# Performance work log

Measured on AMD Instinct MI355X. Metric: run time of the kernel, lower is better.

Reference implementation:

```python
import jax, jax.numpy as jnp
import numpy as np

TAU = 1.0  # temperaturesa
GRID = 5   # torch.chunk(..., 5) along H and W


def _cam(X, gamma, tau):
    # Channel attention: energy = Xf Xf^T over spatial dim, with max-subtraction/negation trick.
    B, C, H, W = X.shape
    Xf = X.reshape(B, C, H * W)
    energy = jnp.einsum('bcn,bdn->bcd', Xf, Xf)                      # [B,C,C]
    energy_new = jnp.max(energy, axis=-1, keepdims=True) - energy
    attn = jax.nn.softmax(energy_new / tau, axis=-1)
    out = jnp.einsum('bcd,bdn->bcn', attn, Xf).reshape(B, C, H, W)
    return gamma * out + X


def _pam(X, Wq, bq, Wk, bk, Wv, bv, gamma, tau):
    # Position attention with 1x1-conv q/k/v (1x1 conv == channel matmul).
    B, C, H, W = X.shape
    N = H * W
    Xf = X.reshape(B, C, N)
    q = jnp.einsum('kc,bcn->bnk', Wq, Xf) + bq                        # [B,N,C//8]
    k = jnp.einsum('kc,bcn->bkn', Wk, Xf) + bk[None, :, None]         # [B,C//8,N]
    v = jnp.einsum('dc,bcn->bdn', Wv, Xf) + bv[None, :, None]         # [B,C,N]
    energy = jnp.einsum('bnk,bkm->bnm', q, k)                         # [B,N,N]
    attn = jax.nn.softmax(energy / tau, axis=-1)
    # torch: bmm(value, attention.permute(0,2,1)) -> out[b,d,m] = sum_n v[b,d,n]*attn[b,m,n]
    out = jnp.einsum('bdn,bmn->bdm', v, attn).reshape(B, C, H, W)
    return gamma * out + X


def _cka_loss(X, Y):
    # linear_CKA_loss: HKH centering done as K - rowmean - colmean + totalmean.
    def cgram(Z):
        K = Z @ Z.T                                                   # [B,B]
        rm = jnp.mean(K, axis=1, keepdims=True)
        cm = jnp.mean(K, axis=0, keepdims=True)
        return K - rm - cm + jnp.mean(K)
    cX, cY = cgram(X), cgram(Y)
    hsic = jnp.sum(cX * cY)
    v1 = jnp.sqrt(jnp.sum(cX * cX))
    v2 = jnp.sqrt(jnp.sum(cY * cY))
    return -jnp.log(jnp.abs(hsic / (v1 * v2)) + 1e-8)


def _grid_chunks(X, g=GRID):
    # 5x5 spatial tiling -> [g*g, B, C, H/g, W/g]
    B, C, H, W = X.shape
    h, w = H // g, W // g
    return X.reshape(B, C, g, h, g, w).transpose(2, 4, 0, 1, 3, 5).reshape(g * g, B, C, h, w)


def setup_inputs() -> dict:
    key = jax.random.key(0)
    ks = jax.random.split(key, 10)
    B, C, H, W = 16, 256, 80, 80
    Ck = C // 8
    return {
        'feat_S': jax.random.normal(ks[0], (B, C, H, W), jnp.float32),
        'feat_T': jax.random.normal(ks[1], (B, C, H, W), jnp.float32),
        'Wq': jax.random.normal(ks[2], (Ck, C), jnp.float32),
        'bq': jax.random.normal(ks[3], (Ck,), jnp.float32),
        'Wk': jax.random.normal(ks[4], (Ck, C), jnp.float32),
        'bk': jax.random.normal(ks[5], (Ck,), jnp.float32),
        'Wv': jax.random.normal(ks[6], (C, C), jnp.float32),
        'bv': jax.random.normal(ks[7], (C,), jnp.float32),
        'gammacam': jax.random.normal(ks[8], (1,), jnp.float32),
        'gammapam': jax.random.normal(ks[9], (1,), jnp.float32),
    }


def reference(feat_S, feat_T, Wq, bq, Wk, bk, Wv, bv, gammacam, gammapam):
    # feature_transform == 'separately_CAMgridPAM_CKA'
    tau = TAU
    pam = lambda X: _pam(X, Wq, bq, Wk, bk, Wv, bv, gammapam, tau)
    chunks_S = _grid_chunks(feat_S)                                   # [25,B,C,16,16]
    chunks_T = _grid_chunks(feat_T)
    pam_S = jax.vmap(pam)(chunks_S)
    pam_T = jax.vmap(pam)(chunks_T)
    nchunk, B = pam_S.shape[0], pam_S.shape[1]
    flat_S = pam_S.reshape(nchunk, B, -1)
    flat_T = pam_T.reshape(nchunk, B, -1)
    loss_PAM = jnp.mean(jax.vmap(_cka_loss)(flat_S, flat_T))          # sum/n == mean
    CAM_S = _cam(feat_S, gammacam, tau)
    CAM_T = _cam(feat_T, gammacam, tau)
    loss_CAM = _cka_loss(CAM_S.reshape(B, -1), CAM_T.reshape(B, -1))
    return (loss_CAM, loss_PAM)
```

## Files before the change

### kernel.cpp

```cpp
#include <hip/hip_runtime.h>


typedef short bf16x8 __attribute__((ext_vector_type(8)));
typedef float f32x4 __attribute__((ext_vector_type(4)));

constexpr int BB = 16;
constexpr int CH = 256;
constexpr int HW = 6400;
constexpr int IMW = 80;

__device__ __forceinline__ int lds_off(int row, int half, int k2) {
  return row * 128 + ((((half << 6)) | k2) ^ ((row & 7) << 4));
}

__device__ __forceinline__ bf16x8 frag_ld(const char* base, int row, int half, int lane) {
  int off = row * 128 + ((((half << 6)) | ((lane >> 4) << 4)) ^ ((lane & 7) << 4));
  return *(const bf16x8*)(base + off);
}

__device__ __forceinline__ void cvt2(float x, unsigned short& h, unsigned short& l) {
  unsigned u = __float_as_uint(x);
  h = (unsigned short)(u >> 16);
  float r = x - __uint_as_float(u & 0xffff0000u);
  l = (unsigned short)(__float_as_uint(r) >> 16);
}

__device__ __forceinline__ void cvt4(float4 v, ushort4& h, ushort4& l) {
  cvt2(v.x, h.x, l.x); cvt2(v.y, h.y, l.y);
  cvt2(v.z, h.z, l.z); cvt2(v.w, h.w, l.w);
}

__device__ __forceinline__ void cvt8(float4 v0, float4 v1, bf16x8& hi, bf16x8& lo) {
  unsigned short h, l;
  cvt2(v0.x, h, l); hi[0] = (short)h; lo[0] = (short)l;
  cvt2(v0.y, h, l); hi[1] = (short)h; lo[1] = (short)l;
  cvt2(v0.z, h, l); hi[2] = (short)h; lo[2] = (short)l;
  cvt2(v0.w, h, l); hi[3] = (short)h; lo[3] = (short)l;
  cvt2(v1.x, h, l); hi[4] = (short)h; lo[4] = (short)l;
  cvt2(v1.y, h, l); hi[5] = (short)h; lo[5] = (short)l;
  cvt2(v1.z, h, l); hi[6] = (short)h; lo[6] = (short)l;
  cvt2(v1.w, h, l); hi[7] = (short)h; lo[7] = (short)l;
}

__device__ __forceinline__ unsigned short bf_rnd(float x) {
  unsigned u = __float_as_uint(x);
  return (unsigned short)((u + 0x8000u) >> 16);
}

__global__ __launch_bounds__(1024) void cam_energy_k(const float* __restrict__ fS,
                                                     const float* __restrict__ fT,
                                                     float* __restrict__ part) {
  const int kc = blockIdx.x, b = blockIdx.y, t = blockIdx.z;
  const float* X = (t ? fT : fS) + (size_t)b * CH * HW;
  __shared__ unsigned short lds[2 * 256 * 64];
  const int tid = threadIdx.x, lane = tid & 63, w = tid >> 6;
  const int wr = w >> 2, wc = w & 3;
  const int r0 = tid >> 2, kq = tid & 3;
  const int half = kq >> 1, k2b = (kq & 1) * 32;
  const float* Xr = X + (size_t)r0 * HW + kc * 800 + kq * 16;
  f32x4 acc[4][4] = {};
  float4 v[4];
#pragma unroll
  for (int q = 0; q < 4; ++q) v[q] = *(const float4*)(Xr + q * 4);
  for (int it = 0; it < 13; ++it) {
    char* pb = (char*)lds + (it & 1) * 32768;
#pragma unroll
    for (int q = 0; q < 4; ++q) {
      ushort4 u;
      u.x = bf_rnd(v[q].x); u.y = bf_rnd(v[q].y);
      u.z = bf_rnd(v[q].z); u.w = bf_rnd(v[q].w);
      *(ushort4*)(pb + lds_off(r0, half, k2b + q * 8)) = u;
    }
    __syncthreads();
    float4 nv[4];
    if (it < 12) {
      const int nk = (it + 1) * 64;
      if (nk + kq * 16 < 800) {
        const float* Xn = Xr + nk;
#pragma unroll
        for (int q = 0; q < 4; ++q) nv[q] = *(const float4*)(Xn + q * 4);
      } else {
#pragma unroll
        for (int q = 0; q < 4; ++q) nv[q] = make_float4(0.f, 0.f, 0.f, 0.f);
      }
    }
#pragma unroll
    for (int h = 0; h < 2; ++h) {
      bf16x8 bh[4];
#pragma unroll
      for (int n = 0; n < 4; ++n)
        bh[n] = frag_ld(pb, wc * 64 + n * 16 + (lane & 15), h, lane);
#pragma unroll
      for (int m = 0; m < 4; ++m) {
        bf16x8 a = frag_ld(pb, wr * 64 + m * 16 + (lane & 15), h, lane);
#pragma unroll
        for (int n = 0; n < 4; ++n)
          acc[m][n] = __builtin_amdgcn_mfma_f32_16x16x32_bf16(a, bh[n], acc[m][n], 0, 0, 0);
      }
    }
#pragma unroll
    for (int q = 0; q < 4; ++q) v[q] = nv[q];
  }
  float* Eb = part + (((size_t)kc * 2 + t) * BB + b) * 65536;
#pragma unroll
  for (int m = 0; m < 4; ++m)
#pragma unroll
    for (int n = 0; n < 4; ++n) {
      int row = wr * 64 + m * 16 + ((lane >> 4) << 2);
      int col = wc * 64 + n * 16 + (lane & 15);
#pragma unroll
      for (int r2 = 0; r2 < 4; ++r2)
        Eb[(size_t)(row + r2) * 256 + col] = acc[m][n][r2];
    }
}

__global__ __launch_bounds__(64) void cam_softmax_k(float* __restrict__ part) {
  const int c = blockIdx.x, b = blockIdx.y, t = blockIdx.z;
  const size_t base = (((size_t)t * BB + b) * CH + c) * CH;
  const int lane = threadIdx.x;
  float4 x = make_float4(0.f, 0.f, 0.f, 0.f);
#pragma unroll
  for (int p = 0; p < 8; ++p) {
    float4 y = ((const float4*)(part + (size_t)p * 2097152 + base))[lane];
    x.x += y.x; x.y += y.y; x.z += y.z; x.w += y.w;
  }
  float mn = fminf(fminf(x.x, x.y), fminf(x.z, x.w));
  for (int o = 32; o; o >>= 1) mn = fminf(mn, __shfl_xor(mn, o));
  float4 p4;
  p4.x = __expf(mn - x.x); p4.y = __expf(mn - x.y);
  p4.z = __expf(mn - x.z); p4.w = __expf(mn - x.w);
  float s = (p4.x + p4.y) + (p4.z + p4.w);
  for (int o = 32; o; o >>= 1) s += __shfl_xor(s, o);
  const float inv = 1.0f / s;
  p4.x *= inv; p4.y *= inv; p4.z *= inv; p4.w *= inv;
  ((float4*)(part + base))[lane] = p4;
}

template <int MODE>
__global__ __launch_bounds__(1024) void ax_k(const float* __restrict__ Abase, int Astride,
                                             const float* __restrict__ X,
                                             float* __restrict__ OUT,
                                             const float* __restrict__ bvec,
                                             const float* __restrict__ gsc) {
  const int nt = blockIdx.x;
  const int b = blockIdx.y;
  const float* A = Abase + (size_t)b * Astride;
  const float* Xb = X + (size_t)b * CH * HW;
  float* OUTb = OUT + (size_t)b * CH * HW;
  const int nbase = nt * 128;
  __shared__ unsigned short lds[2 * (256 + 128) * 64];
  const int tid = threadIdx.x, lane = tid & 63, w = tid >> 6;
  const int wr = w >> 2, wc = w & 3;
  const int r0 = tid >> 2, kq = tid & 3;
  const int n_r = tid & 127, kg = tid >> 7;
  const float* Xcol = Xb + nbase + n_r;
  f32x4 acc[4][2] = {};
  float4 ra[2];
  float vb4[4];
#pragma unroll
  for (int q = 0; q < 2; ++q)
    ra[q] = *(const float4*)(A + (size_t)r0 * 256 + kq * 8 + q * 4);
#pragma unroll
  for (int e = 0; e < 4; ++e)
    vb4[e] = Xcol[(size_t)(kg * 4 + e) * HW];
  for (int s = 0; s < 8; ++s) {
    char* Ab = (char*)lds + (s & 1) * 49152;
    char* Bb = Ab + 32768;
#pragma unroll
    for (int q = 0; q < 2; ++q) {
      ushort4 h4, l4;
      cvt4(ra[q], h4, l4);
      *(ushort4*)(Ab + lds_off(r0, 0, kq * 16 + q * 8)) = h4;
      *(ushort4*)(Ab + lds_off(r0, 1, kq * 16 + q * 8)) = l4;
    }
    {
      unsigned short bh[4], bl[4];
#pragma unroll
      for (int e = 0; e < 4; ++e) cvt2(vb4[e], bh[e], bl[e]);
      *(ushort4*)(Bb + lds_off(n_r, 0, kg * 8)) = make_ushort4(bh[0], bh[1], bh[2], bh[3]);
      *(ushort4*)(Bb + lds_off(n_r, 1, kg * 8)) = make_ushort4(bl[0], bl[1], bl[2], bl[3]);
    }
    __syncthreads();
    if (s < 7) {
      int k0 = (s + 1) * 32;
#pragma unroll
      for (int q = 0; q < 2; ++q)
        ra[q] = *(const float4*)(A + (size_t)r0 * 256 + k0 + kq * 8 + q * 4);
#pragma unroll
      for (int e = 0; e < 4; ++e)
        vb4[e] = Xcol[(size_t)(k0 + kg * 4 + e) * HW];
    }
    bf16x8 bfr[2][2];
#pragma unroll
    for (int h = 0; h < 2; ++h)
#pragma unroll
      for (int n = 0; n < 2; ++n)
        bfr[h][n] = frag_ld(Bb, wc * 32 + n * 16 + (lane & 15), h, lane);
#pragma unroll
    for (int m = 0; m < 4; ++m) {
      int arow = wr * 64 + m * 16 + (lane & 15);
      bf16x8 a0 = frag_ld(Ab, arow, 0, lane);
      bf16x8 a1 = frag_ld(Ab, arow, 1, lane);
#pragma unroll
      for (int n = 0; n < 2; ++n)
        acc[m][n] = __builtin_amdgcn_mfma_f32_16x16x32_bf16(a0, bfr[0][n], acc[m][n], 0, 0, 0);
#pragma unroll
      for (int n = 0; n < 2; ++n)
        acc[m][n] = __builtin_amdgcn_mfma_f32_16x16x32_bf16(a0, bfr[1][n], acc[m][n], 0, 0, 0);
#pragma unroll
      for (int n = 0; n < 2; ++n)
        acc[m][n] = __builtin_amdgcn_mfma_f32_16x16x32_bf16(a1, bfr[0][n], acc[m][n], 0, 0, 0);
    }
  }
  float g = 0.f;
  if (MODE == 0) g = gsc[0];
#pragma unroll
  for (int m = 0; m < 4; ++m)
#pragma unroll
    for (int n = 0; n < 2; ++n) {
      int row = wr * 64 + m * 16 + ((lane >> 4) << 2);
      int col = nbase + wc * 32 + n * 16 + (lane & 15);
#pragma unroll
      for (int r2 = 0; r2 < 4; ++r2) {
        size_t o = (size_t)(row + r2) * HW + col;
        float v = acc[m][n][r2];
        if (MODE == 0) OUTb[o] = g * v + Xb[o];
        else           OUTb[o] = v + bvec[row + r2];
      }
    }
}

__global__ __launch_bounds__(256) void qk_k(const float* __restrict__ X,
                                            const float* __restrict__ Wq,
                                            const float* __restrict__ bq,
                                            const float* __restrict__ Wk,
                                            const float* __restrict__ bk,
                                            float* __restrict__ qt,
                                            float* __restrict__ kf) {
  const int nbase = blockIdx.x * 256;
  const int b = blockIdx.y;
  const float* Xb = X + (size_t)b * CH * HW;
  __shared__ unsigned short lds[(64 + 256) * 64];
  char* Ab = (char*)lds;
  char* Bb = (char*)lds + 8192;
  const int tid = threadIdx.x, lane = tid & 63, w = tid >> 6;
  const int ar = tid >> 2, akq = tid & 3;
  const int n4 = (tid & 63) * 4, c0l = tid >> 6;
  const float* Arow = (ar < 32) ? (Wq + (size_t)ar * CH) : (Wk + (size_t)(ar - 32) * CH);
  f32x4 acc[4][4] = {};
  float4 va[2], vb[8];
#pragma unroll
  for (int q = 0; q < 2; ++q)
    va[q] = *(const float4*)(Arow + akq * 8 + q * 4);
#pragma unroll
  for (int q = 0; q < 8; ++q)
    vb[q] = *(const float4*)(Xb + (size_t)(c0l + 4 * q) * HW + nbase + n4);
  for (int s = 0; s < 8; ++s) {
    __syncthreads();
#pragma unroll
    for (int q = 0; q < 2; ++q) {
      ushort4 h4, l4;
      cvt4(va[q], h4, l4);
      *(ushort4*)(Ab + lds_off(ar, 0, akq * 16 + q * 8)) = h4;
      *(ushort4*)(Ab + lds_off(ar, 1, akq * 16 + q * 8)) = l4;
    }
#pragma unroll
    for (int q = 0; q < 8; ++q) {
      int cc = c0l + 4 * q;
      float4 v = vb[q];
#pragma unroll
      for (int jj = 0; jj < 4; ++jj) {
        int j = (jj + tid) & 3;
        float e = (j == 0) ? v.x : (j == 1) ? v.y : (j == 2) ? v.z : v.w;
        unsigned short h, l;
        cvt2(e, h, l);
        int row = n4 + j;
        *(unsigned short*)(Bb + lds_off(row, 0, cc * 2)) = h;
        *(unsigned short*)(Bb + lds_off(row, 1, cc * 2)) = l;
      }
    }
    __syncthreads();
    float4 na[2], nb[8];
    if (s < 7) {
      const int k0 = (s + 1) * 32;
#pragma unroll
      for (int q = 0; q < 2; ++q)
        na[q] = *(const float4*)(Arow + k0 + akq * 8 + q * 4);
#pragma unroll
      for (int q = 0; q < 8; ++q)
        nb[q] = *(const float4*)(Xb + (size_t)(k0 + c0l + 4 * q) * HW + nbase + n4);
    }
    bf16x8 bfr[2][4];
#pragma unroll
    for (int h = 0; h < 2; ++h)
#pragma unroll
      for (int n = 0; n < 4; ++n)
        bfr[h][n] = frag_ld(Bb, w * 64 + n * 16 + (lane & 15), h, lane);
#pragma unroll
    for (int m = 0; m < 4; ++m) {
      int arow2 = m * 16 + (lane & 15);
      bf16x8 a0 = frag_ld(Ab, arow2, 0, lane);
      bf16x8 a1 = frag_ld(Ab, arow2, 1, lane);
#pragma unroll
      for (int n = 0; n < 4; ++n)
        acc[m][n] = __builtin_amdgcn_mfma_f32_16x16x32_bf16(a0, bfr[0][n], acc[m][n], 0, 0, 0);
#pragma unroll
      for (int n = 0; n < 4; ++n)
        acc[m][n] = __builtin_amdgcn_mfma_f32_16x16x32_bf16(a0, bfr[1][n], acc[m][n], 0, 0, 0);
#pragma unroll
      for (int n = 0; n < 4; ++n)
        acc[m][n] = __builtin_amdgcn_mfma_f32_16x16x32_bf16(a1, bfr[0][n], acc[m][n], 0, 0, 0);
    }
#pragma unroll
    for (int q = 0; q < 2; ++q) va[q] = na[q];
#pragma unroll
    for (int q = 0; q < 8; ++q) vb[q] = nb[q];
  }
#pragma unroll
  for (int m = 0; m < 4; ++m)
#pragma unroll
    for (int n = 0; n < 4; ++n) {
      int row = m * 16 + ((lane >> 4) << 2);
      int col = nbase + w * 64 + n * 16 + (lane & 15);
#pragma unroll
      for (int r2 = 0; r2 < 4; ++r2) {
        int rr = row + r2;
        float v = acc[m][n][r2];
        if (rr < 32) qt[((size_t)b * HW + col) * 32 + rr] = v + bq[rr];
        else         kf[((size_t)b * 32 + (rr - 32)) * HW + col] = v + bk[rr - 32];
      }
    }
}

__global__ __launch_bounds__(256) void pam_es_k(const float* __restrict__ qt,
                                                const float* __restrict__ kf,
                                                float* __restrict__ Pbuf) {
  const int ccb = blockIdx.x;
  const int ck = ccb >> 4, b = ccb & 15;
  const int gi = ck / 5, gj = ck % 5;
  const int pbase = gi * 16 * IMW + gj * 16;
  float* Pc = Pbuf + (size_t)ccb * 65536;
  __shared__ float qs[256][32];
  __shared__ float S[32][256];
  const int tid = threadIdx.x;
  const float* qb = qt + (size_t)b * HW * 32;
#pragma unroll
  for (int qq = 0; qq < 8; ++qq) {
    int j = (tid >> 3) + 32 * qq;
    int nj = pbase + (j >> 4) * IMW + (j & 15);
    float4 v = *(const float4*)(qb + (size_t)nj * 32 + (tid & 7) * 4);
    *(float4*)&qs[j][(tid & 7) * 4] = v;
  }
  const int nt = pbase + (tid >> 4) * IMW + (tid & 15);
  const float* kb = kf + (size_t)b * 32 * HW;
  float kc[32];
#pragma unroll
  for (int kk = 0; kk < 32; ++kk) kc[kk] = kb[(size_t)kk * HW + nt];
  __syncthreads();
  const int w = tid >> 6, lane = tid & 63;
  for (int p = 0; p < 8; ++p) {
#pragma unroll 4
    for (int j2 = 0; j2 < 32; ++j2) {
      int row = p * 32 + j2;
      float s = 0.f;
#pragma unroll
      for (int k8 = 0; k8 < 8; ++k8) {
        float4 qv = *(const float4*)&qs[row][k8 * 4];
        s = fmaf(qv.x, kc[k8 * 4 + 0], s);
        s = fmaf(qv.y, kc[k8 * 4 + 1], s);
        s = fmaf(qv.z, kc[k8 * 4 + 2], s);
        s = fmaf(qv.w, kc[k8 * 4 + 3], s);
      }
      S[j2][tid] = s;
    }
    __syncthreads();
#pragma unroll
    for (int rr = 0; rr < 8; ++rr) {
      int jj = w * 8 + rr;
      float4 v = *(const float4*)&S[jj][lane << 2];
      float m = fmaxf(fmaxf(v.x, v.y), fmaxf(v.z, v.w));
      for (int o = 32; o; o >>= 1) m = fmaxf(m, __shfl_xor(m, o));
      float4 pv;
      pv.x = __expf(v.x - m); pv.y = __expf(v.y - m);
      pv.z = __expf(v.z - m); pv.w = __expf(v.w - m);
      float s = (pv.x + pv.y) + (pv.z + pv.w);
      for (int o = 32; o; o >>= 1) s += __shfl_xor(s, o);
      const float inv = 1.f / s;
      pv.x *= inv; pv.y *= inv; pv.z *= inv; pv.w *= inv;
      *(float4*)&Pc[(size_t)(p * 32 + jj) * 256 + (lane << 2)] = pv;
    }
    __syncthreads();
  }
}

__global__ __launch_bounds__(1024) void pam_pv_k(float* __restrict__ P,
                                                 const float* __restrict__ V,
                                                 const float* __restrict__ fS,
                                                 const float* __restrict__ fT,
                                                 const float* __restrict__ gsc, int t) {
  const int ccb = blockIdx.x;
  const int ck = ccb >> 4, b = ccb & 15;
  const int gi = ck / 5, gj = ck % 5;
  const float* Xb = (t ? fT : fS) + (size_t)b * CH * HW;
  const float* Vb = V + (size_t)b * CH * HW;
  float* Pc = P + (size_t)ccb * 65536;
  __shared__ unsigned short lds[2 * 2 * 256 * 64];
  const int tid = threadIdx.x, lane = tid & 63, w = tid >> 6;
  const int wr = w >> 2, wc = w & 3;
  const int r0 = tid >> 2, kq = tid & 3;
  const int pbase = gi * 16 * IMW + gj * 16;
  f32x4 acc[4][4] = {};
  float4 va[2], vb[2];
  {
    int jj = kq * 8;
    int ngl = pbase + (jj >> 4) * IMW + (jj & 15);
    va[0] = *(const float4*)(Vb + (size_t)r0 * HW + ngl);
    va[1] = *(const float4*)(Vb + (size_t)r0 * HW + ngl + 4);
    vb[0] = *(const float4*)(Pc + (size_t)r0 * 256 + jj);
    vb[1] = *(const float4*)(Pc + (size_t)r0 * 256 + jj + 4);
  }
  for (int s = 0; s < 8; ++s) {
    char* Ab = (char*)lds + (s & 1) * 65536;
    char* Bb = Ab + 32768;
    {
      ushort4 h4, l4;
      cvt4(va[0], h4, l4);
      *(ushort4*)(Ab + lds_off(r0, 0, kq * 16)) = h4;
      *(ushort4*)(Ab + lds_off(r0, 1, kq * 16)) = l4;
      cvt4(va[1], h4, l4);
      *(ushort4*)(Ab + lds_off(r0, 0, kq * 16 + 8)) = h4;
      *(ushort4*)(Ab + lds_off(r0, 1, kq * 16 + 8)) = l4;
      cvt4(vb[0], h4, l4);
      *(ushort4*)(Bb + lds_off(r0, 0, kq * 16)) = h4;
      *(ushort4*)(Bb + lds_off(r0, 1, kq * 16)) = l4;
      cvt4(vb[1], h4, l4);
      *(ushort4*)(Bb + lds_off(r0, 0, kq * 16 + 8)) = h4;
      *(ushort4*)(Bb + lds_off(r0, 1, kq * 16 + 8)) = l4;
    }
    __syncthreads();
    if (s < 7) {
      int k0 = (s + 1) * 32;
      int jj = k0 + kq * 8;
      int ngl = pbase + (jj >> 4) * IMW + (jj & 15);
      va[0] = *(const float4*)(Vb + (size_t)r0 * HW + ngl);
      va[1] = *(const float4*)(Vb + (size_t)r0 * HW + ngl + 4);
      vb[0] = *(const float4*)(Pc + (size_t)r0 * 256 + k0 + kq * 8);
      vb[1] = *(const float4*)(Pc + (size_t)r0 * 256 + k0 + kq * 8 + 4);
    }
#pragma unroll
    for (int hb = 0; hb < 2; ++hb) {
      bf16x8 bh[4];
#pragma unroll
      for (int n = 0; n < 4; ++n)
        bh[n] = frag_ld(Bb, wc * 64 + n * 16 + (lane & 15), hb, lane);
#pragma unroll
      for (int m = 0; m < 4; ++m) {
        int arow = wr * 64 + m * 16 + (lane & 15);
        bf16x8 a0 = frag_ld(Ab, arow, 0, lane);
#pragma unroll
        for (int n = 0; n < 4; ++n)
          acc[m][n] = __builtin_amdgcn_mfma_f32_16x16x32_bf16(a0, bh[n], acc[m][n], 0, 0, 0);
        if (hb == 0) {
          bf16x8 a1 = frag_ld(Ab, arow, 1, lane);
#pragma unroll
          for (int n = 0; n < 4; ++n)
            acc[m][n] = __builtin_amdgcn_mfma_f32_16x16x32_bf16(a1, bh[n], acc[m][n], 0, 0, 0);
        }
      }
    }
  }
  const float g = gsc[0];
#pragma unroll
  for (int m = 0; m < 4; ++m)
#pragma unroll
    for (int n = 0; n < 4; ++n) {
      int row = wr * 64 + m * 16 + ((lane >> 4) << 2);
      int col = wc * 64 + n * 16 + (lane & 15);
      int ngl = pbase + (col >> 4) * IMW + (col & 15);
#pragma unroll
      for (int r2 = 0; r2 < 4; ++r2) {
        float v = g * acc[m][n][r2] + Xb[(size_t)(row + r2) * HW + ngl];
        Pc[(size_t)(row + r2) * 256 + col] = v;
      }
    }
}

__global__ __launch_bounds__(256) void gram_mfma_k(const float* __restrict__ Z,
                                                   size_t gStride, size_t bStride,
                                                   double* __restrict__ G) {
  const int tid = threadIdx.x, lane = tid & 63, w = tid >> 6;
  const float* Zg = Z + (size_t)blockIdx.y * gStride;
  const float* p = Zg + (size_t)(lane & 15) * bStride +
                   (size_t)blockIdx.x * 4096 + w * 1024 + ((lane >> 4) << 3);
  f32x4 acc = {};
#pragma unroll 4
  for (int s = 0; s < 32; ++s) {
    float4 v0 = *(const float4*)(p + s * 32);
    float4 v1 = *(const float4*)(p + s * 32 + 4);
    bf16x8 hi, lo;
    cvt8(v0, v1, hi, lo);
    acc = __builtin_amdgcn_mfma_f32_16x16x32_bf16(hi, hi, acc, 0, 0, 0);
    acc = __builtin_amdgcn_mfma_f32_16x16x32_bf16(hi, lo, acc, 0, 0, 0);
    acc = __builtin_amdgcn_mfma_f32_16x16x32_bf16(lo, hi, acc, 0, 0, 0);
  }
  double* Gt = G + (size_t)blockIdx.y * 256;
  const int col = lane & 15, row0 = (lane >> 4) << 2;
#pragma unroll
  for (int i = 0; i < 4; ++i)
    atomicAdd(&Gt[(size_t)(row0 + i) * 16 + col], (double)acc[i]);
}

__global__ __launch_bounds__(256) void cka_pair_k(const double* __restrict__ G,
                                                  double* __restrict__ losses) {
  const int q = blockIdx.x;
  const double* KX = (q == 0) ? G : G + 512 + (size_t)(q - 1) * 256;
  const double* KY = (q == 0) ? G + 256 : G + 512 + 6400 + (size_t)(q - 1) * 256;
  __shared__ double red[256];
  __shared__ double srm[16], scm[16];
  __shared__ double stm;
  const int tid = threadIdx.x;
  const int r = tid >> 4, c = tid & 15;

  auto center = [&](double k) -> double {
    red[tid] = k;
    __syncthreads();
    for (int off = 8; off; off >>= 1) {
      if (c < off) red[tid] += red[tid + off];
      __syncthreads();
    }
    if (c == 0) srm[r] = red[tid] * (1.0 / 16.0);
    __syncthreads();
    red[c * 16 + r] = k;
    __syncthreads();
    for (int off = 8; off; off >>= 1) {
      if (r < off) red[c * 16 + r] += red[c * 16 + r + off];
      __syncthreads();
    }
    if (r == 0) scm[c] = red[c * 16] * (1.0 / 16.0);
    __syncthreads();
    if (tid == 0) {
      double s = 0.0;
      for (int i = 0; i < 16; ++i) s += srm[i];
      stm = s * (1.0 / 16.0);
    }
    __syncthreads();
    double v = k - srm[r] - scm[c] + stm;
    __syncthreads();
    return v;
  };
  auto reduce_sum = [&](double v) -> double {
    red[tid] = v;
    __syncthreads();
    for (int off = 128; off; off >>= 1) {
      if (tid < off) red[tid] += red[tid + off];
      __syncthreads();
    }
    double s = red[0];
    __syncthreads();
    return s;
  };
  double cx = center(KX[tid]);
  double cy = center(KY[tid]);
  double h = reduce_sum(cx * cy);
  double v1 = reduce_sum(cx * cx);
  double v2 = reduce_sum(cy * cy);
  if (tid == 0) losses[q] = -log(fabs(h / (sqrt(v1) * sqrt(v2))) + 1e-8);
}

__global__ void cka_combine_k(const double* __restrict__ losses,
                              float* __restrict__ out) {
  if (threadIdx.x == 0) {
    out[0] = (float)losses[0];
    double s = 0.0;
    for (int q = 1; q <= 25; ++q) s += losses[q];
    out[1] = (float)(s * (1.0 / 25.0));
  }
}

extern "C" void kernel_launch(void* const* d_in, const int* in_sizes, int n_in,
                              void* d_out, int out_size, void* d_ws, size_t ws_size,
                              hipStream_t stream) {
  (void)in_sizes; (void)n_in; (void)out_size; (void)ws_size;
  const float* fS = (const float*)d_in[0];
  const float* fT = (const float*)d_in[1];
  const float* Wq = (const float*)d_in[2];
  const float* bq = (const float*)d_in[3];
  const float* Wk = (const float*)d_in[4];
  const float* bk = (const float*)d_in[5];
  const float* Wv = (const float*)d_in[6];
  const float* bv = (const float*)d_in[7];
  const float* gcam = (const float*)d_in[8];
  const float* gpam = (const float*)d_in[9];
  float* out = (float*)d_out;

  float* buf0 = (float*)d_ws;
  float* buf1 = buf0 + 26214400;
  double* G = (double*)(buf1 + 26214400);
  float* Pbuf = buf1;
  float* qt = buf0;
  float* kf = buf0 + 3276800;
  double* losses = (double*)buf0;

  hipMemsetAsync(G, 0, 13312 * sizeof(double), stream);

  cam_energy_k<<<dim3(8, 16, 2), 1024, 0, stream>>>(fS, fT, buf1);
  cam_softmax_k<<<dim3(256, 16, 2), 64, 0, stream>>>(buf1);
  for (int t = 0; t < 2; ++t) {
    ax_k<0><<<dim3(50, 16), 1024, 0, stream>>>(buf1 + (size_t)t * BB * 65536, 65536,
                                               t ? fT : fS, buf0, nullptr, gcam);
    gram_mfma_k<<<dim3(400, 1), 256, 0, stream>>>(buf0, (size_t)0, (size_t)1638400,
                                                  G + t * 256);
  }
  for (int t = 0; t < 2; ++t) {
    const float* X = t ? fT : fS;
    qk_k<<<dim3(25, 16), 256, 0, stream>>>(X, Wq, bq, Wk, bk, qt, kf);
    pam_es_k<<<dim3(400), 256, 0, stream>>>(qt, kf, Pbuf);
    ax_k<1><<<dim3(50, 16), 1024, 0, stream>>>(Wv, 0, X, buf0, bv, nullptr);
    pam_pv_k<<<dim3(400), 1024, 0, stream>>>(Pbuf, buf0, fS, fT, gpam, t);
    gram_mfma_k<<<dim3(16, 25), 256, 0, stream>>>(Pbuf, (size_t)1048576, (size_t)65536,
                                                  G + 512 + t * 6400);
  }
  cka_pair_k<<<dim3(26), 256, 0, stream>>>(G, losses);
  cka_combine_k<<<dim3(1), 64, 0, stream>>>(losses, out);
}
```

Before: 993.5 us.

## Shrink GEMM blocks to 512 threads, single LDS buffer, split PV output columns

ax_k and pam_pv_k now run 512-thread blocks (launch bounds 512,4), with each wave computing a 64x64 tile. The LDS double buffer is replaced by a single buffer guarded by two barriers per k-step, so less shared memory is used per block and more blocks can reside on a CU. pam_pv_k is split into two blocks per chunk, one per half of the output positions, and writes its result in a per-half layout. That layout is a consistent permutation across S and T, so the later Gram computation is unaffected. The intent is to raise occupancy and parallelism, at the cost of losing the overlap between LDS writes and MFMA work and adding an extra barrier per step.

```diff
diff --git a/kernel.cpp b/kernel.cpp
--- a/kernel.cpp
+++ b/kernel.cpp
@@ -137,79 +137,82 @@
 }
 
 template <int MODE>
-__global__ __launch_bounds__(1024) void ax_k(const float* __restrict__ Abase, int Astride,
-                                             const float* __restrict__ X,
-                                             float* __restrict__ OUT,
-                                             const float* __restrict__ bvec,
-                                             const float* __restrict__ gsc) {
+__global__ __launch_bounds__(512, 4) void ax_k(const float* __restrict__ Abase, int Astride,
+                                               const float* __restrict__ X,
+                                               float* __restrict__ OUT,
+                                               const float* __restrict__ bvec,
+                                               const float* __restrict__ gsc) {
   const int nt = blockIdx.x;
   const int b = blockIdx.y;
   const float* A = Abase + (size_t)b * Astride;
   const float* Xb = X + (size_t)b * CH * HW;
   float* OUTb = OUT + (size_t)b * CH * HW;
   const int nbase = nt * 128;
-  __shared__ unsigned short lds[2 * (256 + 128) * 64];
+  __shared__ unsigned short lds[(256 + 128) * 64];
+  char* Ab = (char*)lds;
+  char* Bb = (char*)lds + 32768;
   const int tid = threadIdx.x, lane = tid & 63, w = tid >> 6;
-  const int wr = w >> 2, wc = w & 3;
-  const int r0 = tid >> 2, kq = tid & 3;
+  const int wr = w >> 1, wc = w & 1;
+  const int r0a = tid >> 1, kqa = tid & 1;
   const int n_r = tid & 127, kg = tid >> 7;
   const float* Xcol = Xb + nbase + n_r;
-  f32x4 acc[4][2] = {};
-  float4 ra[2];
-  float vb4[4];
-#pragma unroll
-  for (int q = 0; q < 2; ++q)
-    ra[q] = *(const float4*)(A + (size_t)r0 * 256 + kq * 8 + q * 4);
-#pragma unroll
-  for (int e = 0; e < 4; ++e)
-    vb4[e] = Xcol[(size_t)(kg * 4 + e) * HW];
+  f32x4 acc[4][4] = {};
+  float4 ra[4];
+  float vb8[8];
+#pragma unroll
+  for (int q = 0; q < 4; ++q)
+    ra[q] = *(const float4*)(A + (size_t)r0a * 256 + kqa * 16 + q * 4);
+#pragma unroll
+  for (int e = 0; e < 8; ++e)
+    vb8[e] = Xcol[(size_t)(kg * 8 + e) * HW];
   for (int s = 0; s < 8; ++s) {
-    char* Ab = (char*)lds + (s & 1) * 49152;
-    char* Bb = Ab + 32768;
-#pragma unroll
-    for (int q = 0; q < 2; ++q) {
+    __syncthreads();
+#pragma unroll
+    for (int q = 0; q < 4; ++q) {
       ushort4 h4, l4;
       cvt4(ra[q], h4, l4);
-      *(ushort4*)(Ab + lds_off(r0, 0, kq * 16 + q * 8)) = h4;
-      *(ushort4*)(Ab + lds_off(r0, 1, kq * 16 + q * 8)) = l4;
+      *(ushort4*)(Ab + lds_off(r0a, 0, kqa * 32 + q * 8)) = h4;
+      *(ushort4*)(Ab + lds_off(r0a, 1, kqa * 32 + q * 8)) = l4;
     }
     {
-      unsigned short bh[4], bl[4];
-#pragma unroll
-      for (int e = 0; e < 4; ++e) cvt2(vb4[e], bh[e], bl[e]);
-      *(ushort4*)(Bb + lds_off(n_r, 0, kg * 8)) = make_ushort4(bh[0], bh[1], bh[2], bh[3]);
-      *(ushort4*)(Bb + lds_off(n_r, 1, kg * 8)) = make_ushort4(bl[0], bl[1], bl[2], bl[3]);
+      unsigned short bh[8], bl[8];
+#pragma unroll
+      for (int e = 0; e < 8; ++e) cvt2(vb8[e], bh[e], bl[e]);
+      *(ushort4*)(Bb + lds_off(n_r, 0, kg * 16)) = make_ushort4(bh[0], bh[1], bh[2], bh[3]);
+      *(ushort4*)(Bb + lds_off(n_r, 0, kg * 16 + 8)) = make_ushort4(bh[4], bh[5], bh[6], bh[7]);
+      *(ushort4*)(Bb + lds_off(n_r, 1, kg * 16)) = make_ushort4(bl[0], bl[1], bl[2], bl[3]);
+      *(ushort4*)(Bb + lds_off(n_r, 1, kg * 16 + 8)) = make_ushort4(bl[4], bl[5], bl[6], bl[7]);
     }
     __syncthreads();
     if (s < 7) {
       int k0 = (s + 1) * 32;
 #pragma unroll
-      for (int q = 0; q < 2; ++q)
-        ra[q] = *(const float4*)(A + (size_t)r0 * 256 + k0 + kq * 8 + q * 4);
-#pragma unroll
-      for (int e = 0; e < 4; ++e)
-        vb4[e] = Xcol[(size_t)(k0 + kg * 4 + e) * HW];
-    }
-    bf16x8 bfr[2][2];
-#pragma unroll
-    for (int h = 0; h < 2; ++h)
-#pragma unroll
-      for (int n = 0; n < 2; ++n)
-        bfr[h][n] = frag_ld(Bb, wc * 32 + n * 16 + (lane & 15), h, lane);
-#pragma unroll
-    for (int m = 0; m < 4; ++m) {
-      int arow = wr * 64 + m * 16 + (lane & 15);
-      bf16x8 a0 = frag_ld(Ab, arow, 0, lane);
-      bf16x8 a1 = frag_ld(Ab, arow, 1, lane);
-#pragma unroll
-      for (int n = 0; n < 2; ++n)
-        acc[m][n] = __builtin_amdgcn_mfma_f32_16x16x32_bf16(a0, bfr[0][n], acc[m][n], 0, 0, 0);
-#pragma unroll
-      for (int n = 0; n < 2; ++n)
-        acc[m][n] = __builtin_amdgcn_mfma_f32_16x16x32_bf16(a0, bfr[1][n], acc[m][n], 0, 0, 0);
-#pragma unroll
-      for (int n = 0; n < 2; ++n)
-        acc[m][n] = __builtin_amdgcn_mfma_f32_16x16x32_bf16(a1, bfr[0][n], acc[m][n], 0, 0, 0);
+      for (int q = 0; q < 4; ++q)
+        ra[q] = *(const float4*)(A + (size_t)r0a * 256 + k0 + kqa * 16 + q * 4);
+#pragma unroll
+      for (int e = 0; e < 8; ++e)
+        vb8[e] = Xcol[(size_t)(k0 + kg * 8 + e) * HW];
+    }
+#pragma unroll
+    for (int hb = 0; hb < 2; ++hb) {
+      bf16x8 bh[4];
+#pragma unroll
+      for (int n = 0; n < 4; ++n)
+        bh[n] = frag_ld(Bb, wc * 64 + n * 16 + (lane & 15), hb, lane);
+#pragma unroll
+      for (int m = 0; m < 4; ++m) {
+        int arow = wr * 64 + m * 16 + (lane & 15);
+        bf16x8 a0 = frag_ld(Ab, arow, 0, lane);
+#pragma unroll
+        for (int n = 0; n < 4; ++n)
+          acc[m][n] = __builtin_amdgcn_mfma_f32_16x16x32_bf16(a0, bh[n], acc[m][n], 0, 0, 0);
+        if (hb == 0) {
+          bf16x8 a1 = frag_ld(Ab, arow, 1, lane);
+#pragma unroll
+          for (int n = 0; n < 4; ++n)
+            acc[m][n] = __builtin_amdgcn_mfma_f32_16x16x32_bf16(a1, bh[n], acc[m][n], 0, 0, 0);
+        }
+      }
     }
   }
   float g = 0.f;
@@ -217,9 +220,9 @@
 #pragma unroll
   for (int m = 0; m < 4; ++m)
 #pragma unroll
-    for (int n = 0; n < 2; ++n) {
+    for (int n = 0; n < 4; ++n) {
       int row = wr * 64 + m * 16 + ((lane >> 4) << 2);
-      int col = nbase + wc * 32 + n * 16 + (lane & 15);
+      int col = nbase + wc * 64 + n * 16 + (lane & 15);
 #pragma unroll
       for (int r2 = 0; r2 < 4; ++r2) {
         size_t o = (size_t)(row + r2) * HW + col;
@@ -393,59 +396,67 @@
   }
 }
 
-__global__ __launch_bounds__(1024) void pam_pv_k(float* __restrict__ P,
-                                                 const float* __restrict__ V,
-                                                 const float* __restrict__ fS,
-                                                 const float* __restrict__ fT,
-                                                 const float* __restrict__ gsc, int t) {
-  const int ccb = blockIdx.x;
+__global__ __launch_bounds__(512, 4) void pam_pv_k(float* __restrict__ P,
+                                                   const float* __restrict__ V,
+                                                   const float* __restrict__ fS,
+                                                   const float* __restrict__ fT,
+                                                   const float* __restrict__ gsc, int t) {
+  const int jh = blockIdx.x;
+  const int ccb = blockIdx.y;
   const int ck = ccb >> 4, b = ccb & 15;
   const int gi = ck / 5, gj = ck % 5;
   const float* Xb = (t ? fT : fS) + (size_t)b * CH * HW;
   const float* Vb = V + (size_t)b * CH * HW;
   float* Pc = P + (size_t)ccb * 65536;
-  __shared__ unsigned short lds[2 * 2 * 256 * 64];
+  const float* Pr = Pc + (size_t)jh * 32768;
+  float* Oc = Pc + (size_t)jh * 32768;
+  __shared__ unsigned short lds[(256 + 128) * 64];
+  char* Ab = (char*)lds;
+  char* Bb = (char*)lds + 32768;
   const int tid = threadIdx.x, lane = tid & 63, w = tid >> 6;
-  const int wr = w >> 2, wc = w & 3;
-  const int r0 = tid >> 2, kq = tid & 3;
+  const int wr = w >> 1, wc = w & 1;
+  const int r0a = tid >> 1, kqa = tid & 1;
+  const int r0b = tid >> 2, kqb = tid & 3;
   const int pbase = gi * 16 * IMW + gj * 16;
   f32x4 acc[4][4] = {};
-  float4 va[2], vb[2];
+  float4 va[4], vp[2];
   {
-    int jj = kq * 8;
-    int ngl = pbase + (jj >> 4) * IMW + (jj & 15);
-    va[0] = *(const float4*)(Vb + (size_t)r0 * HW + ngl);
-    va[1] = *(const float4*)(Vb + (size_t)r0 * HW + ngl + 4);
-    vb[0] = *(const float4*)(Pc + (size_t)r0 * 256 + jj);
-    vb[1] = *(const float4*)(Pc + (size_t)r0 * 256 + jj + 4);
+    int jj = kqa * 16;
+    int ngl = pbase + (jj >> 4) * IMW;
+#pragma unroll
+    for (int q = 0; q < 4; ++q)
+      va[q] = *(const float4*)(Vb + (size_t)r0a * HW + ngl + q * 4);
+#pragma unroll
+    for (int q = 0; q < 2; ++q)
+      vp[q] = *(const float4*)(Pr + (size_t)r0b * 256 + kqb * 8 + q * 4);
   }
   for (int s = 0; s < 8; ++s) {
-    char* Ab = (char*)lds + (s & 1) * 65536;
-    char* Bb = Ab + 32768;
-    {
+    __syncthreads();
+#pragma unroll
+    for (int q = 0; q < 4; ++q) {
       ushort4 h4, l4;
-      cvt4(va[0], h4, l4);
-      *(ushort4*)(Ab + lds_off(r0, 0, kq * 16)) = h4;
-      *(ushort4*)(Ab + lds_off(r0, 1, kq * 16)) = l4;
-      cvt4(va[1], h4, l4);
-      *(ushort4*)(Ab + lds_off(r0, 0, kq * 16 + 8)) = h4;
-      *(ushort4*)(Ab + lds_off(r0, 1, kq * 16 + 8)) = l4;
-      cvt4(vb[0], h4, l4);
-      *(ushort4*)(Bb + lds_off(r0, 0, kq * 16)) = h4;
-      *(ushort4*)(Bb + lds_off(r0, 1, kq * 16)) = l4;
-      cvt4(vb[1], h4, l4);
-      *(ushort4*)(Bb + lds_off(r0, 0, kq * 16 + 8)) = h4;
-      *(ushort4*)(Bb + lds_off(r0, 1, kq * 16 + 8)) = l4;
+      cvt4(va[q], h4, l4);
+      *(ushort4*)(Ab + lds_off(r0a, 0, kqa * 32 + q * 8)) = h4;
+      *(ushort4*)(Ab + lds_off(r0a, 1, kqa * 32 + q * 8)) = l4;
+    }
+#pragma unroll
+    for (int q = 0; q < 2; ++q) {
+      ushort4 h4, l4;
+      cvt4(vp[q], h4, l4);
+      *(ushort4*)(Bb + lds_off(r0b, 0, kqb * 16 + q * 8)) = h4;
+      *(ushort4*)(Bb + lds_off(r0b, 1, kqb * 16 + q * 8)) = l4;
     }
     __syncthreads();
     if (s < 7) {
       int k0 = (s + 1) * 32;
-      int jj = k0 + kq * 8;
-      int ngl = pbase + (jj >> 4) * IMW + (jj & 15);
-      va[0] = *(const float4*)(Vb + (size_t)r0 * HW + ngl);
-      va[1] = *(const float4*)(Vb + (size_t)r0 * HW + ngl + 4);
-      vb[0] = *(const float4*)(Pc + (size_t)r0 * 256 + k0 + kq * 8);
-      vb[1] = *(const float4*)(Pc + (size_t)r0 * 256 + k0 + kq * 8 + 4);
+      int jj = k0 + kqa * 16;
+      int ngl = pbase + (jj >> 4) * IMW;
+#pragma unroll
+      for (int q = 0; q < 4; ++q)
+        va[q] = *(const float4*)(Vb + (size_t)r0a * HW + ngl + q * 4);
+#pragma unroll
+      for (int q = 0; q < 2; ++q)
+        vp[q] = *(const float4*)(Pr + (size_t)r0b * 256 + k0 + kqb * 8 + q * 4);
     }
 #pragma unroll
     for (int hb = 0; hb < 2; ++hb) {
@@ -475,12 +486,13 @@
 #pragma unroll
     for (int n = 0; n < 4; ++n) {
       int row = wr * 64 + m * 16 + ((lane >> 4) << 2);
-      int col = wc * 64 + n * 16 + (lane & 15);
-      int ngl = pbase + (col >> 4) * IMW + (col & 15);
+      int jloc = wc * 64 + n * 16 + (lane & 15);
+      int jg = jh * 128 + jloc;
+      int ngl = pbase + (jg >> 4) * IMW + (jg & 15);
 #pragma unroll
       for (int r2 = 0; r2 < 4; ++r2) {
         float v = g * acc[m][n][r2] + Xb[(size_t)(row + r2) * HW + ngl];
-        Pc[(size_t)(row + r2) * 256 + col] = v;
+        Oc[(size_t)(row + r2) * 128 + jloc] = v;
       }
     }
 }
@@ -606,8 +618,8 @@
   cam_energy_k<<<dim3(8, 16, 2), 1024, 0, stream>>>(fS, fT, buf1);
   cam_softmax_k<<<dim3(256, 16, 2), 64, 0, stream>>>(buf1);
   for (int t = 0; t < 2; ++t) {
-    ax_k<0><<<dim3(50, 16), 1024, 0, stream>>>(buf1 + (size_t)t * BB * 65536, 65536,
-                                               t ? fT : fS, buf0, nullptr, gcam);
+    ax_k<0><<<dim3(50, 16), 512, 0, stream>>>(buf1 + (size_t)t * BB * 65536, 65536,
+                                              t ? fT : fS, buf0, nullptr, gcam);
     gram_mfma_k<<<dim3(400, 1), 256, 0, stream>>>(buf0, (size_t)0, (size_t)1638400,
                                                   G + t * 256);
   }
@@ -615,8 +627,8 @@
     const float* X = t ? fT : fS;
     qk_k<<<dim3(25, 16), 256, 0, stream>>>(X, Wq, bq, Wk, bk, qt, kf);
     pam_es_k<<<dim3(400), 256, 0, stream>>>(qt, kf, Pbuf);
-    ax_k<1><<<dim3(50, 16), 1024, 0, stream>>>(Wv, 0, X, buf0, bv, nullptr);
-    pam_pv_k<<<dim3(400), 1024, 0, stream>>>(Pbuf, buf0, fS, fT, gpam, t);
+    ax_k<1><<<dim3(50, 16), 512, 0, stream>>>(Wv, 0, X, buf0, bv, nullptr);
+    pam_pv_k<<<dim3(2, 400), 512, 0, stream>>>(Pbuf, buf0, fS, fT, gpam, t);
     gram_mfma_k<<<dim3(16, 25), 256, 0, stream>>>(Pbuf, (size_t)1048576, (size_t)65536,
                                                   G + 512 + t * 6400);
   }
```

New measurement: 1.071 ms. 1.08x slower.

## Halve ax_k block size with larger per-wave tiles and single-buffered LDS

Applied to the files above, without the earlier changes.

The channel-mixing GEMM kernel ax_k now runs 512 threads per block instead of 1024. Each wave computes a 64x64 output tile (4x4 MFMA accumulators) instead of 64x32, and each thread stages more A and X elements. LDS drops from double-buffered to single-buffered with an extra barrier at the top of each k-step, which cuts shared memory per block so that up to 4 blocks fit per CU. The aim is more fragment reuse per LDS load and higher occupancy, at the cost of more registers per thread and losing the overlap that double buffering gave.

```diff
diff --git a/kernel.cpp b/kernel.cpp
--- a/kernel.cpp
+++ b/kernel.cpp
@@ -137,79 +137,82 @@
 }
 
 template <int MODE>
-__global__ __launch_bounds__(1024) void ax_k(const float* __restrict__ Abase, int Astride,
-                                             const float* __restrict__ X,
-                                             float* __restrict__ OUT,
-                                             const float* __restrict__ bvec,
-                                             const float* __restrict__ gsc) {
+__global__ __launch_bounds__(512, 4) void ax_k(const float* __restrict__ Abase, int Astride,
+                                               const float* __restrict__ X,
+                                               float* __restrict__ OUT,
+                                               const float* __restrict__ bvec,
+                                               const float* __restrict__ gsc) {
   const int nt = blockIdx.x;
   const int b = blockIdx.y;
   const float* A = Abase + (size_t)b * Astride;
   const float* Xb = X + (size_t)b * CH * HW;
   float* OUTb = OUT + (size_t)b * CH * HW;
   const int nbase = nt * 128;
-  __shared__ unsigned short lds[2 * (256 + 128) * 64];
+  __shared__ unsigned short lds[(256 + 128) * 64];
+  char* Ab = (char*)lds;
+  char* Bb = (char*)lds + 32768;
   const int tid = threadIdx.x, lane = tid & 63, w = tid >> 6;
-  const int wr = w >> 2, wc = w & 3;
-  const int r0 = tid >> 2, kq = tid & 3;
+  const int wr = w >> 1, wc = w & 1;
+  const int r0a = tid >> 1, kqa = tid & 1;
   const int n_r = tid & 127, kg = tid >> 7;
   const float* Xcol = Xb + nbase + n_r;
-  f32x4 acc[4][2] = {};
-  float4 ra[2];
-  float vb4[4];
-#pragma unroll
-  for (int q = 0; q < 2; ++q)
-    ra[q] = *(const float4*)(A + (size_t)r0 * 256 + kq * 8 + q * 4);
-#pragma unroll
-  for (int e = 0; e < 4; ++e)
-    vb4[e] = Xcol[(size_t)(kg * 4 + e) * HW];
+  f32x4 acc[4][4] = {};
+  float4 ra[4];
+  float vb8[8];
+#pragma unroll
+  for (int q = 0; q < 4; ++q)
+    ra[q] = *(const float4*)(A + (size_t)r0a * 256 + kqa * 16 + q * 4);
+#pragma unroll
+  for (int e = 0; e < 8; ++e)
+    vb8[e] = Xcol[(size_t)(kg * 8 + e) * HW];
   for (int s = 0; s < 8; ++s) {
-    char* Ab = (char*)lds + (s & 1) * 49152;
-    char* Bb = Ab + 32768;
-#pragma unroll
-    for (int q = 0; q < 2; ++q) {
+    __syncthreads();
+#pragma unroll
+    for (int q = 0; q < 4; ++q) {
       ushort4 h4, l4;
       cvt4(ra[q], h4, l4);
-      *(ushort4*)(Ab + lds_off(r0, 0, kq * 16 + q * 8)) = h4;
-      *(ushort4*)(Ab + lds_off(r0, 1, kq * 16 + q * 8)) = l4;
+      *(ushort4*)(Ab + lds_off(r0a, 0, kqa * 32 + q * 8)) = h4;
+      *(ushort4*)(Ab + lds_off(r0a, 1, kqa * 32 + q * 8)) = l4;
     }
     {
-      unsigned short bh[4], bl[4];
-#pragma unroll
-      for (int e = 0; e < 4; ++e) cvt2(vb4[e], bh[e], bl[e]);
-      *(ushort4*)(Bb + lds_off(n_r, 0, kg * 8)) = make_ushort4(bh[0], bh[1], bh[2], bh[3]);
-      *(ushort4*)(Bb + lds_off(n_r, 1, kg * 8)) = make_ushort4(bl[0], bl[1], bl[2], bl[3]);
+      unsigned short bh[8], bl[8];
+#pragma unroll
+      for (int e = 0; e < 8; ++e) cvt2(vb8[e], bh[e], bl[e]);
+      *(ushort4*)(Bb + lds_off(n_r, 0, kg * 16)) = make_ushort4(bh[0], bh[1], bh[2], bh[3]);
+      *(ushort4*)(Bb + lds_off(n_r, 0, kg * 16 + 8)) = make_ushort4(bh[4], bh[5], bh[6], bh[7]);
+      *(ushort4*)(Bb + lds_off(n_r, 1, kg * 16)) = make_ushort4(bl[0], bl[1], bl[2], bl[3]);
+      *(ushort4*)(Bb + lds_off(n_r, 1, kg * 16 + 8)) = make_ushort4(bl[4], bl[5], bl[6], bl[7]);
     }
     __syncthreads();
     if (s < 7) {
       int k0 = (s + 1) * 32;
 #pragma unroll
-      for (int q = 0; q < 2; ++q)
-        ra[q] = *(const float4*)(A + (size_t)r0 * 256 + k0 + kq * 8 + q * 4);
-#pragma unroll
-      for (int e = 0; e < 4; ++e)
-        vb4[e] = Xcol[(size_t)(k0 + kg * 4 + e) * HW];
-    }
-    bf16x8 bfr[2][2];
-#pragma unroll
-    for (int h = 0; h < 2; ++h)
-#pragma unroll
-      for (int n = 0; n < 2; ++n)
-        bfr[h][n] = frag_ld(Bb, wc * 32 + n * 16 + (lane & 15), h, lane);
-#pragma unroll
-    for (int m = 0; m < 4; ++m) {
-      int arow = wr * 64 + m * 16 + (lane & 15);
-      bf16x8 a0 = frag_ld(Ab, arow, 0, lane);
-      bf16x8 a1 = frag_ld(Ab, arow, 1, lane);
-#pragma unroll
-      for (int n = 0; n < 2; ++n)
-        acc[m][n] = __builtin_amdgcn_mfma_f32_16x16x32_bf16(a0, bfr[0][n], acc[m][n], 0, 0, 0);
-#pragma unroll
-      for (int n = 0; n < 2; ++n)
-        acc[m][n] = __builtin_amdgcn_mfma_f32_16x16x32_bf16(a0, bfr[1][n], acc[m][n], 0, 0, 0);
-#pragma unroll
-      for (int n = 0; n < 2; ++n)
-        acc[m][n] = __builtin_amdgcn_mfma_f32_16x16x32_bf16(a1, bfr[0][n], acc[m][n], 0, 0, 0);
+      for (int q = 0; q < 4; ++q)
+        ra[q] = *(const float4*)(A + (size_t)r0a * 256 + k0 + kqa * 16 + q * 4);
+#pragma unroll
+      for (int e = 0; e < 8; ++e)
+        vb8[e] = Xcol[(size_t)(k0 + kg * 8 + e) * HW];
+    }
+#pragma unroll
+    for (int hb = 0; hb < 2; ++hb) {
+      bf16x8 bh[4];
+#pragma unroll
+      for (int n = 0; n < 4; ++n)
+        bh[n] = frag_ld(Bb, wc * 64 + n * 16 + (lane & 15), hb, lane);
+#pragma unroll
+      for (int m = 0; m < 4; ++m) {
+        int arow = wr * 64 + m * 16 + (lane & 15);
+        bf16x8 a0 = frag_ld(Ab, arow, 0, lane);
+#pragma unroll
+        for (int n = 0; n < 4; ++n)
+          acc[m][n] = __builtin_amdgcn_mfma_f32_16x16x32_bf16(a0, bh[n], acc[m][n], 0, 0, 0);
+        if (hb == 0) {
+          bf16x8 a1 = frag_ld(Ab, arow, 1, lane);
+#pragma unroll
+          for (int n = 0; n < 4; ++n)
+            acc[m][n] = __builtin_amdgcn_mfma_f32_16x16x32_bf16(a1, bh[n], acc[m][n], 0, 0, 0);
+        }
+      }
     }
   }
   float g = 0.f;
@@ -217,9 +220,9 @@
 #pragma unroll
   for (int m = 0; m < 4; ++m)
 #pragma unroll
-    for (int n = 0; n < 2; ++n) {
+    for (int n = 0; n < 4; ++n) {
       int row = wr * 64 + m * 16 + ((lane >> 4) << 2);
-      int col = nbase + wc * 32 + n * 16 + (lane & 15);
+      int col = nbase + wc * 64 + n * 16 + (lane & 15);
 #pragma unroll
       for (int r2 = 0; r2 < 4; ++r2) {
         size_t o = (size_t)(row + r2) * HW + col;
@@ -606,8 +609,8 @@
   cam_energy_k<<<dim3(8, 16, 2), 1024, 0, stream>>>(fS, fT, buf1);
   cam_softmax_k<<<dim3(256, 16, 2), 64, 0, stream>>>(buf1);
   for (int t = 0; t < 2; ++t) {
-    ax_k<0><<<dim3(50, 16), 1024, 0, stream>>>(buf1 + (size_t)t * BB * 65536, 65536,
-                                               t ? fT : fS, buf0, nullptr, gcam);
+    ax_k<0><<<dim3(50, 16), 512, 0, stream>>>(buf1 + (size_t)t * BB * 65536, 65536,
+                                              t ? fT : fS, buf0, nullptr, gcam);
     gram_mfma_k<<<dim3(400, 1), 256, 0, stream>>>(buf0, (size_t)0, (size_t)1638400,
                                                   G + t * 256);
   }
@@ -615,7 +618,7 @@
     const float* X = t ? fT : fS;
     qk_k<<<dim3(25, 16), 256, 0, stream>>>(X, Wq, bq, Wk, bk, qt, kf);
     pam_es_k<<<dim3(400), 256, 0, stream>>>(qt, kf, Pbuf);
-    ax_k<1><<<dim3(50, 16), 1024, 0, stream>>>(Wv, 0, X, buf0, bv, nullptr);
+    ax_k<1><<<dim3(50, 16), 512, 0, stream>>>(Wv, 0, X, buf0, bv, nullptr);
     pam_pv_k<<<dim3(400), 1024, 0, stream>>>(Pbuf, buf0, fS, fT, gpam, t);
     gram_mfma_k<<<dim3(16, 25), 256, 0, stream>>>(Pbuf, (size_t)1048576, (size_t)65536,
                                                   G + 512 + t * 6400);
```

New measurement: 1.017 ms. +2.4%, slower.
